# Performance work log

Measured on AMD Instinct MI355X. Metric: run time of the kernel, lower is better.

The kernel has to match this reference:

```python
import jax, jax.numpy as jnp
import numpy as np

T, B, IN, H = 256, 128, 512, 1024


def setup_inputs() -> dict:
    key = jax.random.key(0)
    ks = jax.random.split(key, 13)
    s = 1.0 / float(np.sqrt(H))  # torch LSTMCell init: U(-1/sqrt(H), 1/sqrt(H))
    u = lambda k, shp: jax.random.uniform(k, shp, jnp.float32, -s, s)
    return {
        "x": jax.random.normal(ks[0], (T, B, IN), jnp.float32),
        "h0_fwd": jax.random.normal(ks[1], (B, H), jnp.float32),
        "c0_fwd": jax.random.normal(ks[2], (B, H), jnp.float32),
        "h0_rev": jax.random.normal(ks[3], (B, H), jnp.float32),
        "c0_rev": jax.random.normal(ks[4], (B, H), jnp.float32),
        "W_ih_f": u(ks[5], (4 * H, IN)),
        "W_hh_f": u(ks[6], (4 * H, H)),
        "b_ih_f": u(ks[7], (4 * H,)),
        "b_hh_f": u(ks[8], (4 * H,)),
        "W_ih_r": u(ks[9], (4 * H, IN)),
        "W_hh_r": u(ks[10], (4 * H, H)),
        "b_ih_r": u(ks[11], (4 * H,)),
        "b_hh_r": u(ks[12], (4 * H,)),
    }


def _lstm(x, h0, c0, Wih, Whh, bih, bhh, reverse):
    # Precompute the input projection for all timesteps in one big GEMM.
    xp = jnp.einsum('tbi,gi->tbg', x, Wih) + bih + bhh  # [T, B, 4H]

    def step(carry, xg):
        h, c = carry
        gates = xg + h @ Whh.T  # [B, 4H]
        i, f, g, o = jnp.split(gates, 4, axis=-1)  # torch gate order: i, f, g, o
        c = jax.nn.sigmoid(f) * c + jax.nn.sigmoid(i) * jnp.tanh(g)
        h = jax.nn.sigmoid(o) * jnp.tanh(c)
        return (h, c), h

    # reverse=True scans backward in time but emits outputs in original order,
    # exactly matching ReverseLSTMLayer's reverse-process-then-reverse-outputs.
    (h, c), ys = jax.lax.scan(step, (h0, c0), xp, reverse=reverse)
    return ys, h, c


def reference(x, h0_fwd, c0_fwd, h0_rev, c0_rev,
              W_ih_f, W_hh_f, b_ih_f, b_hh_f,
              W_ih_r, W_hh_r, b_ih_r, b_hh_r):
    yf, hf, cf = _lstm(x, h0_fwd, c0_fwd, W_ih_f, W_hh_f, b_ih_f, b_hh_f, False)
    yr, hr, cr = _lstm(x, h0_rev, c0_rev, W_ih_r, W_hh_r, b_ih_r, b_hh_r, True)
    out = jnp.concatenate([yf, yr], axis=-1)  # [T, B, 2H]
    # Faithful to the original's `hidden, cell = output_states` quirk:
    # `hidden` is the forward direction's (h, c) pair stacked,
    # `cell` is the reverse direction's (h, c) pair stacked.
    hidden = jnp.stack([hf, cf])  # [2, B, H]
    cell = jnp.stack([hr, cr])    # [2, B, H]
    return out, (hidden, cell)
```

## Files before the change

kernel.cpp:

```cpp
#include <hip/hip_runtime.h>
#include <hip/hip_bf16.h>

typedef unsigned short u16;
typedef __attribute__((ext_vector_type(8))) short bf16x8;
typedef __attribute__((ext_vector_type(8))) u16   u16x8;
typedef __attribute__((ext_vector_type(4))) float f32x4;

#define T_STEPS 256
#define BATCH   128
#define INDIM   512
#define HDIM    1024
#define GDIM    4096
#define KTOT    1536

#define OFF_XBF   ((size_t)0)
#define XBF_BYTES ((size_t)T_STEPS * BATCH * INDIM * 2)
#define OFF_BM    (OFF_XBF + XBF_BYTES)
#define BM_BYTES  ((size_t)2 * GDIM * KTOT * 2)
#define OFF_BIAS  (OFF_BM + BM_BYTES)
#define BIAS_BYTES ((size_t)2 * GDIM * 4)
#define OFF_CNT   (OFF_BIAS + BIAS_BYTES)
#define OFF_ROLL  (OFF_CNT + 8192)
#define ROLL_BYTES ((size_t)(T_STEPS + 1) * 2 * BATCH * HDIM * 2)
#define WS_NEED   (OFF_ROLL + ROLL_BYTES)


__device__ __forceinline__ u16 f2b(float f) {
  __hip_bfloat16 h = __float2bfloat16(f);
  return *reinterpret_cast<u16*>(&h);
}

__global__ void k_cast_x(const float* __restrict__ x, u16* __restrict__ xs) {
  int i = blockIdx.x * 256 + threadIdx.x;
  int t   = i >> 13;
  int r13 = i & 8191;
  int row = r13 >> 6;
  int c0  = (r13 & 63) * 8;
  int mt = row >> 6, rloc = row & 63;
  int mi = rloc >> 4, ar = rloc & 15;
  int kq = c0 >> 7, ksx = (c0 >> 5) & 3, h4 = (c0 & 31) >> 3;
  const float* src = x + ((size_t)t * BATCH + row) * INDIM + c0;
  f32x4 a = *reinterpret_cast<const f32x4*>(src);
  f32x4 b = *reinterpret_cast<const f32x4*>(src + 4);
  u16x8 u;
  u[0] = f2b(a[0]); u[1] = f2b(a[1]); u[2] = f2b(a[2]); u[3] = f2b(a[3]);
  u[4] = f2b(b[0]); u[5] = f2b(b[1]); u[6] = f2b(b[2]); u[7] = f2b(b[3]);
  size_t dst = ((size_t)(t * 2 + mt)) * 32768
             + (((size_t)((kq * 4 + ksx) * 4 + mi)) * 64 + h4 * 16 + ar) * 8;
  *reinterpret_cast<u16x8*>(xs + dst) = u;
}

__global__ void k_build_b(const float* __restrict__ Whh_f, const float* __restrict__ Wih_f,
                          const float* __restrict__ Whh_r, const float* __restrict__ Wih_r,
                          u16* __restrict__ Bm) {
  int blk = blockIdx.x;
  int dir = blk >> 6, jt = blk & 63;
  const float* Whh = dir ? Whh_r : Whh_f;
  const float* Wih = dir ? Wih_r : Wih_f;
  u16* dst = Bm + (size_t)blk * 64 * KTOT;
  for (int c = 0; c < 64; c++) {
    int G = (c >> 4) * HDIM + jt * 16 + (c & 15);
    for (int k = threadIdx.x; k < KTOT; k += 256) {
      float v = (k < HDIM) ? Whh[(size_t)G * HDIM + k] : Wih[(size_t)G * INDIM + (k - HDIM)];
      dst[c * KTOT + k] = f2b(v);
    }
  }
}

__global__ void k_init(const float* __restrict__ h0f, const float* __restrict__ h0r,
                       const float* __restrict__ bihf, const float* __restrict__ bhhf,
                       const float* __restrict__ bihr, const float* __restrict__ bhhr,
                       u16* __restrict__ hfrag, float* __restrict__ bias,
                       unsigned* __restrict__ flags) {
  int i = blockIdx.x * 256 + threadIdx.x;
  if (i < 2 * BATCH * HDIM) {
    int dir = i / (BATCH * HDIM);
    int rem = i - dir * BATCH * HDIM;
    int r = rem / HDIM, c = rem - r * HDIM;
    int mt = r >> 6, rloc = r & 63;
    int mi = rloc >> 4, ar = rloc & 15;
    int kq = c >> 8, ks = (c >> 5) & 7, h4 = (c & 31) >> 3, e = c & 7;
    const float* h0 = dir ? h0r : h0f;
    size_t off = ((size_t)(dir * 2 + mt)) * 65536
               + (((size_t)((kq * 8 + ks) * 4 + mi)) * 64 + h4 * 16 + ar) * 8 + e;
    hfrag[off] = f2b(h0[rem]);
  }
  if (i < 2 * GDIM) {
    int dir = i / GDIM, g = i - dir * GDIM;
    bias[i] = dir ? (bihr[g] + bhhr[g]) : (bihf[g] + bhhf[g]);
  }
  if (i < 512) flags[i] = 0;
}

__global__ __launch_bounds__(512, 2) void k_lstm(
    const u16* __restrict__ xs, const u16* __restrict__ Bm,
    u16* __restrict__ hfrag,
    const float* __restrict__ bias, unsigned* __restrict__ flags,
    const float* __restrict__ c0f, const float* __restrict__ c0r,
    float* __restrict__ out) {
  __shared__ char ldsAll[70656 + 65536];
  float* ldsP = reinterpret_cast<float*>(ldsAll);
  char* bxl = ldsAll + 70656;

  __builtin_amdgcn_fence(__ATOMIC_ACQUIRE, "agent");

  const int wg   = blockIdx.x;
  const int xcd  = wg & 7, local = wg >> 3;
  const int grp  = xcd >> 1;
  const int dir  = grp >> 1, mt = grp & 1;
  const int jt   = ((xcd & 1) << 5) | local;
  const int tid  = threadIdx.x;
  const int w = tid >> 6, lane = tid & 63;
  const int kq = w >> 1, nh = w & 1;
  const int h4 = lane >> 4, kk = h4 * 8;
  const int ar = lane & 15;

  const u16* bsrc = Bm + (size_t)(dir * 64 + jt) * 64 * KTOT;
  bf16x8 bh[8][2];
#pragma unroll
  for (int ks = 0; ks < 8; ks++)
#pragma unroll
    for (int ni = 0; ni < 2; ni++)
      bh[ks][ni] = *reinterpret_cast<const bf16x8*>(
          bsrc + (size_t)(nh * 32 + ni * 16 + ar) * KTOT + 256 * kq + 32 * ks + kk);

#pragma unroll
  for (int i = 0; i < 8; i++) {
    int fid = i * 8 + w;
    int kq2 = fid >> 4, ksx2 = (fid >> 2) & 3, nh2 = (fid >> 1) & 1, ni2 = fid & 1;
    bf16x8 v = *reinterpret_cast<const bf16x8*>(
        bsrc + (size_t)(nh2 * 32 + ni2 * 16 + ar) * KTOT + HDIM + 128 * kq2 + 32 * ksx2 + kk);
    *reinterpret_cast<bf16x8*>(bxl + ((size_t)fid * 64 + lane) * 16) = v;
  }

  const int rrow = tid >> 3;
  const int jl0  = 2 * (tid & 7);
  const int row0 = mt * 64 + rrow;
  const int jg0  = jt * 16 + jl0;
  const float* c0 = dir ? c0r : c0f;
  float2 cc = *reinterpret_cast<const float2*>(c0 + (size_t)row0 * HDIM + jg0);
  float cst0 = cc.x, cst1 = cc.y;
  const float2 b_i = *reinterpret_cast<const float2*>(bias + dir * GDIM + 0 * HDIM + jg0);
  const float2 b_f = *reinterpret_cast<const float2*>(bias + dir * GDIM + 1 * HDIM + jg0);
  const float2 b_g = *reinterpret_cast<const float2*>(bias + dir * GDIM + 2 * HDIM + jg0);
  const float2 b_o = *reinterpret_cast<const float2*>(bias + dir * GDIM + 3 * HDIM + jg0);

  const size_t poff = (((size_t)(((jg0 >> 8) * 8 + ((jg0 >> 5) & 7)) * 4 + (rrow >> 4))) * 64
                       + ((jg0 & 31) >> 3) * 16 + (rrow & 15)) * 8 + (jg0 & 7);

  const unsigned* fpw = flags + grp * 64 + 16 * kq + (lane & 15);

  __syncthreads();

#pragma unroll 1
  for (int s = 0; s < T_STEPS; s++) {
    const int t = dir ? (T_STEPS - 1 - s) : s;

    bf16x8 ax[4][4];
    {
      const u16* xb = xs + ((size_t)(t * 2 + mt)) * 32768;
#pragma unroll
      for (int ksx = 0; ksx < 4; ksx++)
#pragma unroll
        for (int mi = 0; mi < 4; mi++)
          ax[ksx][mi] = *reinterpret_cast<const bf16x8*>(
              xb + (((size_t)((kq * 4 + ksx) * 4 + mi)) * 64 + lane) * 8);
    }

    if (s > 0) {
      while (true) {
        unsigned f = __hip_atomic_load(fpw, __ATOMIC_RELAXED, __HIP_MEMORY_SCOPE_AGENT);
        if (__all((int)(f >= (unsigned)s))) break;
        __builtin_amdgcn_s_sleep(1);
      }
      __builtin_amdgcn_sched_barrier(0);
    }

    f32x4 acc[4][2];
#pragma unroll
    for (int mi = 0; mi < 4; mi++)
#pragma unroll
      for (int ni = 0; ni < 2; ni++) acc[mi][ni] = f32x4{0.f, 0.f, 0.f, 0.f};

    const u16* hB = hfrag + ((size_t)(s * 4 + dir * 2 + mt)) * 65536;
    bf16x8 ahA[2][4], ahB[2][4];

#define LOADQ(BUF, G)                                                          \
  {                                                                            \
    _Pragma("unroll")                                                          \
    for (int k2 = 0; k2 < 2; k2++)                                             \
      _Pragma("unroll")                                                        \
      for (int mi = 0; mi < 4; mi++)                                           \
        BUF[k2][mi] = *reinterpret_cast<const bf16x8*>(                        \
            hB + (((size_t)((kq * 8 + 2 * (G) + k2) * 4 + mi)) * 64 + lane) * 8); \
  }
#define MFMAQ(BUF, G)                                                          \
  {                                                                            \
    _Pragma("unroll")                                                          \
    for (int k2 = 0; k2 < 2; k2++)                                             \
      _Pragma("unroll")                                                        \
      for (int mi = 0; mi < 4; mi++)                                           \
        _Pragma("unroll")                                                      \
        for (int ni = 0; ni < 2; ni++)                                         \
          acc[mi][ni] = __builtin_amdgcn_mfma_f32_16x16x32_bf16(               \
              BUF[k2][mi], bh[2 * (G) + k2][ni], acc[mi][ni], 0, 0, 0);        \
  }

    LOADQ(ahA, 0);

#pragma unroll
    for (int ksx = 0; ksx < 4; ksx++) {
      bf16x8 bxf[2];
#pragma unroll
      for (int ni = 0; ni < 2; ni++)
        bxf[ni] = *reinterpret_cast<const bf16x8*>(
            bxl + (((size_t)(((kq * 4 + ksx) * 2 + nh) * 2 + ni)) * 64 + lane) * 16);
#pragma unroll
      for (int mi = 0; mi < 4; mi++)
#pragma unroll
        for (int ni = 0; ni < 2; ni++)
          acc[mi][ni] = __builtin_amdgcn_mfma_f32_16x16x32_bf16(ax[ksx][mi], bxf[ni], acc[mi][ni], 0, 0, 0);
    }

    LOADQ(ahB, 1); MFMAQ(ahA, 0);
    LOADQ(ahA, 2); MFMAQ(ahB, 1);
    LOADQ(ahB, 3); MFMAQ(ahA, 2);
    MFMAQ(ahB, 3);
#undef LOADQ
#undef MFMAQ

    {
      float* pw = ldsP + kq * (64 * 69);
#pragma unroll
      for (int mi = 0; mi < 4; mi++)
#pragma unroll
        for (int ni = 0; ni < 2; ni++) {
          int col = nh * 32 + ni * 16 + ar;
          *reinterpret_cast<f32x4*>(pw + col * 69 + mi * 16 + h4 * 4) = acc[mi][ni];
        }
    }
    __syncthreads();

    float h0v, h1v;
    {
      float gi0 = b_i.x, gi1 = b_i.y, gf0 = b_f.x, gf1 = b_f.y;
      float gg0 = b_g.x, gg1 = b_g.y, go0 = b_o.x, go1 = b_o.y;
#pragma unroll
      for (int k4 = 0; k4 < 4; k4++) {
        const float* p = ldsP + k4 * (64 * 69);
        gi0 += p[(0 * 16 + jl0) * 69 + rrow]; gi1 += p[(0 * 16 + jl0 + 1) * 69 + rrow];
        gf0 += p[(1 * 16 + jl0) * 69 + rrow]; gf1 += p[(1 * 16 + jl0 + 1) * 69 + rrow];
        gg0 += p[(2 * 16 + jl0) * 69 + rrow]; gg1 += p[(2 * 16 + jl0 + 1) * 69 + rrow];
        go0 += p[(3 * 16 + jl0) * 69 + rrow]; go1 += p[(3 * 16 + jl0 + 1) * 69 + rrow];
      }
      float i0 = 1.f / (1.f + __expf(-gi0)), i1 = 1.f / (1.f + __expf(-gi1));
      float f0 = 1.f / (1.f + __expf(-gf0)), f1 = 1.f / (1.f + __expf(-gf1));
      float g0 = tanhf(gg0), g1 = tanhf(gg1);
      float o0 = 1.f / (1.f + __expf(-go0)), o1 = 1.f / (1.f + __expf(-go1));
      cst0 = f0 * cst0 + i0 * g0;
      cst1 = f1 * cst1 + i1 * g1;
      h0v = o0 * tanhf(cst0);
      h1v = o1 * tanhf(cst1);

      unsigned hp = (unsigned)f2b(h0v) | ((unsigned)f2b(h1v) << 16);
      u16* hD = hfrag + ((size_t)((s + 1) * 4 + dir * 2 + mt)) * 65536;
      __hip_atomic_store(reinterpret_cast<unsigned*>(hD + poff),
                         hp, __ATOMIC_RELAXED, __HIP_MEMORY_SCOPE_AGENT);
    }

    asm volatile("s_waitcnt vmcnt(0)" ::: "memory");
    __syncthreads();
    if (tid == 0)
      __hip_atomic_store(flags + grp * 64 + jt, (unsigned)(s + 1),
                         __ATOMIC_RELAXED, __HIP_MEMORY_SCOPE_AGENT);

    {
      float2 yv; yv.x = h0v; yv.y = h1v;
      *reinterpret_cast<float2*>(out + ((size_t)t * BATCH + row0) * (2 * HDIM)
                                     + (size_t)dir * HDIM + jg0) = yv;
      if (s == T_STEPS - 1) {
        size_t hid = (size_t)T_STEPS * BATCH * 2 * HDIM;
        size_t base2 = hid + (size_t)dir * 2 * BATCH * HDIM;
        *reinterpret_cast<float2*>(out + base2 + (size_t)row0 * HDIM + jg0) = yv;
        float2 cv; cv.x = cst0; cv.y = cst1;
        *reinterpret_cast<float2*>(out + base2 + (size_t)BATCH * HDIM
                                       + (size_t)row0 * HDIM + jg0) = cv;
      }
    }
  }
}

extern "C" void kernel_launch(void* const* d_in, const int* in_sizes, int n_in,
                              void* d_out, int out_size, void* d_ws, size_t ws_size,
                              hipStream_t stream) {
  const float* x     = (const float*)d_in[0];
  const float* h0f   = (const float*)d_in[1];
  const float* c0f   = (const float*)d_in[2];
  const float* h0r   = (const float*)d_in[3];
  const float* c0r   = (const float*)d_in[4];
  const float* Wih_f = (const float*)d_in[5];
  const float* Whh_f = (const float*)d_in[6];
  const float* bih_f = (const float*)d_in[7];
  const float* bhh_f = (const float*)d_in[8];
  const float* Wih_r = (const float*)d_in[9];
  const float* Whh_r = (const float*)d_in[10];
  const float* bih_r = (const float*)d_in[11];
  const float* bhh_r = (const float*)d_in[12];
  float* out = (float*)d_out;
  char* ws = (char*)d_ws;

  if (ws_size < WS_NEED) return;

  u16* xsf        = (u16*)(ws + OFF_XBF);
  u16* Bm         = (u16*)(ws + OFF_BM);
  float* bias     = (float*)(ws + OFF_BIAS);
  unsigned* flags = (unsigned*)(ws + OFF_CNT);
  u16* hfrag      = (u16*)(ws + OFF_ROLL);

  k_cast_x<<<8192, 256, 0, stream>>>(x, xsf);
  k_build_b<<<128, 256, 0, stream>>>(Whh_f, Wih_f, Whh_r, Wih_r, Bm);
  k_init<<<1024, 256, 0, stream>>>(h0f, h0r, bih_f, bhh_f, bih_r, bhh_r,
                                   hfrag, bias, flags);
  k_lstm<<<256, 512, 0, stream>>>(xsf, Bm, hfrag, bias, flags, c0f, c0r, out);
}
```

Baseline: 2.270 ms.

## Stage recurrent h tile into LDS via async global_load_lds with XOR swizzle

Each step, the workgroup now copies its full 64x1024 bf16 h tile from the rolling global buffer into LDS using global_load_lds DMA. The copy is issued before the input-projection MFMAs so it overlaps with them. Each wave then reads its A fragments from LDS through an XOR-swizzled row layout instead of issuing per-wave global fragment loads. The W_ih fragments move from LDS into registers, and the weight matrix is pre-laid out in fragment order, which also removes the extra LDS staging of W_ih. The cost is an extra barrier per step, higher register pressure, and the whole 128KB LDS being reused for both the h tile and the partial sums.

```diff
diff --git a/kernel.cpp b/kernel.cpp
--- a/kernel.cpp
+++ b/kernel.cpp
@@ -24,10 +24,15 @@
 #define ROLL_BYTES ((size_t)(T_STEPS + 1) * 2 * BATCH * HDIM * 2)
 #define WS_NEED   (OFF_ROLL + ROLL_BYTES)
 
-
 __device__ __forceinline__ u16 f2b(float f) {
   __hip_bfloat16 h = __float2bfloat16(f);
   return *reinterpret_cast<u16*>(&h);
+}
+
+__device__ __forceinline__ void glds16(const void* g, void* l) {
+  __builtin_amdgcn_global_load_lds(
+      (const __attribute__((address_space(1))) unsigned int*)g,
+      (__attribute__((address_space(3))) unsigned int*)l, 16, 0, 0);
 }
 
 __global__ void k_cast_x(const float* __restrict__ x, u16* __restrict__ xs) {
@@ -57,12 +62,24 @@
   int dir = blk >> 6, jt = blk & 63;
   const float* Whh = dir ? Whh_r : Whh_f;
   const float* Wih = dir ? Wih_r : Wih_f;
-  u16* dst = Bm + (size_t)blk * 64 * KTOT;
+  u16* dst = Bm + (size_t)blk * 98304;
   for (int c = 0; c < 64; c++) {
-    int G = (c >> 4) * HDIM + jt * 16 + (c & 15);
+    int G  = (c >> 4) * HDIM + jt * 16 + (c & 15);
+    int nh = c >> 5, ni = (c >> 4) & 1, ar = c & 15;
     for (int k = threadIdx.x; k < KTOT; k += 256) {
-      float v = (k < HDIM) ? Whh[(size_t)G * HDIM + k] : Wih[(size_t)G * INDIM + (k - HDIM)];
-      dst[c * KTOT + k] = f2b(v);
+      size_t off;
+      float v;
+      if (k < HDIM) {
+        int kq = k >> 8, ks = (k >> 5) & 7, h4 = (k & 31) >> 3, e = k & 7;
+        off = ((((size_t)(kq * 8 + ks) * 2 + nh) * 2 + ni) * 64 + h4 * 16 + ar) * 8 + e;
+        v = Whh[(size_t)G * HDIM + k];
+      } else {
+        int kx = k - HDIM;
+        int kq2 = kx >> 7, ksx = (kx >> 5) & 3, h4 = (kx & 31) >> 3, e = kx & 7;
+        off = 65536 + ((((size_t)(kq2 * 4 + ksx) * 2 + nh) * 2 + ni) * 64 + h4 * 16 + ar) * 8 + e;
+        v = Wih[(size_t)G * INDIM + kx];
+      }
+      dst[off] = f2b(v);
     }
   }
 }
@@ -70,20 +87,17 @@
 __global__ void k_init(const float* __restrict__ h0f, const float* __restrict__ h0r,
                        const float* __restrict__ bihf, const float* __restrict__ bhhf,
                        const float* __restrict__ bihr, const float* __restrict__ bhhr,
-                       u16* __restrict__ hfrag, float* __restrict__ bias,
+                       u16* __restrict__ hroll, float* __restrict__ bias,
                        unsigned* __restrict__ flags) {
   int i = blockIdx.x * 256 + threadIdx.x;
   if (i < 2 * BATCH * HDIM) {
     int dir = i / (BATCH * HDIM);
     int rem = i - dir * BATCH * HDIM;
     int r = rem / HDIM, c = rem - r * HDIM;
-    int mt = r >> 6, rloc = r & 63;
-    int mi = rloc >> 4, ar = rloc & 15;
-    int kq = c >> 8, ks = (c >> 5) & 7, h4 = (c & 31) >> 3, e = c & 7;
     const float* h0 = dir ? h0r : h0f;
-    size_t off = ((size_t)(dir * 2 + mt)) * 65536
-               + (((size_t)((kq * 8 + ks) * 4 + mi)) * 64 + h4 * 16 + ar) * 8 + e;
-    hfrag[off] = f2b(h0[rem]);
+    char* hb = (char*)hroll;
+    *(u16*)(hb + ((size_t)dir * BATCH + r) * 2048 + ((2 * c) ^ ((r & 7) << 4))) =
+        f2b(h0[rem]);
   }
   if (i < 2 * GDIM) {
     int dir = i / GDIM, g = i - dir * GDIM;
@@ -94,13 +108,12 @@
 
 __global__ __launch_bounds__(512, 2) void k_lstm(
     const u16* __restrict__ xs, const u16* __restrict__ Bm,
-    u16* __restrict__ hfrag,
+    u16* __restrict__ hroll,
     const float* __restrict__ bias, unsigned* __restrict__ flags,
     const float* __restrict__ c0f, const float* __restrict__ c0r,
     float* __restrict__ out) {
-  __shared__ char ldsAll[70656 + 65536];
-  float* ldsP = reinterpret_cast<float*>(ldsAll);
-  char* bxl = ldsAll + 70656;
+  __shared__ char ldsc[131072];
+  float* ldsP = reinterpret_cast<float*>(ldsc);
 
   __builtin_amdgcn_fence(__ATOMIC_ACQUIRE, "agent");
 
@@ -115,23 +128,20 @@
   const int h4 = lane >> 4, kk = h4 * 8;
   const int ar = lane & 15;
 
-  const u16* bsrc = Bm + (size_t)(dir * 64 + jt) * 64 * KTOT;
-  bf16x8 bh[8][2];
+  const u16* bp = Bm + (size_t)(dir * 64 + jt) * 98304;
+  bf16x8 bh[8][2], bx[4][2];
 #pragma unroll
   for (int ks = 0; ks < 8; ks++)
 #pragma unroll
     for (int ni = 0; ni < 2; ni++)
       bh[ks][ni] = *reinterpret_cast<const bf16x8*>(
-          bsrc + (size_t)(nh * 32 + ni * 16 + ar) * KTOT + 256 * kq + 32 * ks + kk);
-
-#pragma unroll
-  for (int i = 0; i < 8; i++) {
-    int fid = i * 8 + w;
-    int kq2 = fid >> 4, ksx2 = (fid >> 2) & 3, nh2 = (fid >> 1) & 1, ni2 = fid & 1;
-    bf16x8 v = *reinterpret_cast<const bf16x8*>(
-        bsrc + (size_t)(nh2 * 32 + ni2 * 16 + ar) * KTOT + HDIM + 128 * kq2 + 32 * ksx2 + kk);
-    *reinterpret_cast<bf16x8*>(bxl + ((size_t)fid * 64 + lane) * 16) = v;
-  }
+          bp + ((((size_t)(kq * 8 + ks) * 2 + nh) * 2 + ni) * 64 + lane) * 8);
+#pragma unroll
+  for (int ksx = 0; ksx < 4; ksx++)
+#pragma unroll
+    for (int ni = 0; ni < 2; ni++)
+      bx[ksx][ni] = *reinterpret_cast<const bf16x8*>(
+          bp + 65536 + ((((size_t)(kq * 4 + ksx) * 2 + nh) * 2 + ni) * 64 + lane) * 8);
 
   const int rrow = tid >> 3;
   const int jl0  = 2 * (tid & 7);
@@ -145,12 +155,7 @@
   const float2 b_g = *reinterpret_cast<const float2*>(bias + dir * GDIM + 2 * HDIM + jg0);
   const float2 b_o = *reinterpret_cast<const float2*>(bias + dir * GDIM + 3 * HDIM + jg0);
 
-  const size_t poff = (((size_t)(((jg0 >> 8) * 8 + ((jg0 >> 5) & 7)) * 4 + (rrow >> 4))) * 64
-                       + ((jg0 & 31) >> 3) * 16 + (rrow & 15)) * 8 + (jg0 & 7);
-
-  const unsigned* fpw = flags + grp * 64 + 16 * kq + (lane & 15);
-
-  __syncthreads();
+  const unsigned* fpA = flags + grp * 64 + lane;
 
 #pragma unroll 1
   for (int s = 0; s < T_STEPS; s++) {
@@ -169,65 +174,55 @@
 
     if (s > 0) {
       while (true) {
-        unsigned f = __hip_atomic_load(fpw, __ATOMIC_RELAXED, __HIP_MEMORY_SCOPE_AGENT);
+        unsigned f = __hip_atomic_load(fpA, __ATOMIC_RELAXED, __HIP_MEMORY_SCOPE_AGENT);
         if (__all((int)(f >= (unsigned)s))) break;
         __builtin_amdgcn_s_sleep(1);
       }
       __builtin_amdgcn_sched_barrier(0);
     }
 
+    {
+      const char* hRd = (const char*)(hroll + ((size_t)s * 2 + dir) * BATCH * HDIM
+                                            + (size_t)mt * 64 * HDIM);
+      unsigned off = (unsigned)tid * 16;
+#pragma unroll
+      for (int i = 0; i < 16; i++)
+        glds16(hRd + off + i * 8192, ldsc + off + i * 8192);
+    }
+    __builtin_amdgcn_sched_barrier(0);
+
     f32x4 acc[4][2];
 #pragma unroll
     for (int mi = 0; mi < 4; mi++)
 #pragma unroll
       for (int ni = 0; ni < 2; ni++) acc[mi][ni] = f32x4{0.f, 0.f, 0.f, 0.f};
-
-    const u16* hB = hfrag + ((size_t)(s * 4 + dir * 2 + mt)) * 65536;
-    bf16x8 ahA[2][4], ahB[2][4];
-
-#define LOADQ(BUF, G)                                                          \
-  {                                                                            \
-    _Pragma("unroll")                                                          \
-    for (int k2 = 0; k2 < 2; k2++)                                             \
-      _Pragma("unroll")                                                        \
-      for (int mi = 0; mi < 4; mi++)                                           \
-        BUF[k2][mi] = *reinterpret_cast<const bf16x8*>(                        \
-            hB + (((size_t)((kq * 8 + 2 * (G) + k2) * 4 + mi)) * 64 + lane) * 8); \
-  }
-#define MFMAQ(BUF, G)                                                          \
-  {                                                                            \
-    _Pragma("unroll")                                                          \
-    for (int k2 = 0; k2 < 2; k2++)                                             \
-      _Pragma("unroll")                                                        \
-      for (int mi = 0; mi < 4; mi++)                                           \
-        _Pragma("unroll")                                                      \
-        for (int ni = 0; ni < 2; ni++)                                         \
-          acc[mi][ni] = __builtin_amdgcn_mfma_f32_16x16x32_bf16(               \
-              BUF[k2][mi], bh[2 * (G) + k2][ni], acc[mi][ni], 0, 0, 0);        \
-  }
-
-    LOADQ(ahA, 0);
-
-#pragma unroll
-    for (int ksx = 0; ksx < 4; ksx++) {
-      bf16x8 bxf[2];
-#pragma unroll
-      for (int ni = 0; ni < 2; ni++)
-        bxf[ni] = *reinterpret_cast<const bf16x8*>(
-            bxl + (((size_t)(((kq * 4 + ksx) * 2 + nh) * 2 + ni)) * 64 + lane) * 16);
+#pragma unroll
+    for (int ksx = 0; ksx < 4; ksx++)
 #pragma unroll
       for (int mi = 0; mi < 4; mi++)
 #pragma unroll
         for (int ni = 0; ni < 2; ni++)
-          acc[mi][ni] = __builtin_amdgcn_mfma_f32_16x16x32_bf16(ax[ksx][mi], bxf[ni], acc[mi][ni], 0, 0, 0);
-    }
-
-    LOADQ(ahB, 1); MFMAQ(ahA, 0);
-    LOADQ(ahA, 2); MFMAQ(ahB, 1);
-    LOADQ(ahB, 3); MFMAQ(ahA, 2);
-    MFMAQ(ahB, 3);
-#undef LOADQ
-#undef MFMAQ
+          acc[mi][ni] = __builtin_amdgcn_mfma_f32_16x16x32_bf16(ax[ksx][mi], bx[ksx][ni], acc[mi][ni], 0, 0, 0);
+
+    __syncthreads();
+
+#pragma unroll
+    for (int ks = 0; ks < 8; ks++) {
+      bf16x8 af[4];
+#pragma unroll
+      for (int mi = 0; mi < 4; mi++) {
+        unsigned row = 16 * mi + ar;
+        unsigned cb = (256 * kq + 32 * ks + kk) * 2;
+        af[mi] = *reinterpret_cast<const bf16x8*>(
+            ldsc + row * 2048 + (cb ^ ((row & 7) << 4)));
+      }
+#pragma unroll
+      for (int mi = 0; mi < 4; mi++)
+#pragma unroll
+        for (int ni = 0; ni < 2; ni++)
+          acc[mi][ni] = __builtin_amdgcn_mfma_f32_16x16x32_bf16(af[mi], bh[ks][ni], acc[mi][ni], 0, 0, 0);
+    }
+    __syncthreads();
 
     {
       float* pw = ldsP + kq * (64 * 69);
@@ -263,9 +258,10 @@
       h1v = o1 * tanhf(cst1);
 
       unsigned hp = (unsigned)f2b(h0v) | ((unsigned)f2b(h1v) << 16);
-      u16* hD = hfrag + ((size_t)((s + 1) * 4 + dir * 2 + mt)) * 65536;
-      __hip_atomic_store(reinterpret_cast<unsigned*>(hD + poff),
-                         hp, __ATOMIC_RELAXED, __HIP_MEMORY_SCOPE_AGENT);
+      char* hb = (char*)(hroll + ((size_t)(s + 1) * 2 + dir) * BATCH * HDIM);
+      __hip_atomic_store(
+          (unsigned*)(hb + (size_t)row0 * 2048 + ((2 * jg0) ^ ((row0 & 7) << 4))),
+          hp, __ATOMIC_RELAXED, __HIP_MEMORY_SCOPE_AGENT);
     }
 
     asm volatile("s_waitcnt vmcnt(0)" ::: "memory");
@@ -315,11 +311,11 @@
   u16* Bm         = (u16*)(ws + OFF_BM);
   float* bias     = (float*)(ws + OFF_BIAS);
   unsigned* flags = (unsigned*)(ws + OFF_CNT);
-  u16* hfrag      = (u16*)(ws + OFF_ROLL);
+  u16* hroll      = (u16*)(ws + OFF_ROLL);
 
   k_cast_x<<<8192, 256, 0, stream>>>(x, xsf);
   k_build_b<<<128, 256, 0, stream>>>(Whh_f, Wih_f, Whh_r, Wih_r, Bm);
   k_init<<<1024, 256, 0, stream>>>(h0f, h0r, bih_f, bhh_f, bih_r, bhh_r,
-                                   hfrag, bias, flags);
-  k_lstm<<<256, 512, 0, stream>>>(xsf, Bm, hfrag, bias, flags, c0f, c0r, out);
-}
+                                   hroll, bias, flags);
+  k_lstm<<<256, 512, 0, stream>>>(xsf, Bm, hroll, bias, flags, c0f, c0r, out);
+}
```

Result: faster. 2.180 ms (-4.0%).
